# Performance work log

Measured on AMD Instinct MI355X. Metric: run time of the kernel, lower is better.

## Reference

```python
import jax, jax.numpy as jnp
import numpy as np

SR = 8                      # search_range
MO = 2 * SR + 1             # max_offset = 17
NC = MO * MO                # 289 cost-volume channels


def _l2_normalize(x, eps=1e-12):
    # torch F.normalize(p=2, dim=1): x / max(||x||_2, eps)
    n = jnp.sqrt(jnp.sum(x * x, axis=1, keepdims=True))
    return x / jnp.maximum(n, eps)


def _conv2d(x, w, b, pad, groups=1):
    out = jax.lax.conv_general_dilated(
        x, w, window_strides=(1, 1), padding=[(pad, pad), (pad, pad)],
        feature_group_count=groups,
        dimension_numbers=('NCHW', 'OIHW', 'NCHW'))
    return out + b[None, :, None, None]


def _cost_volume(x1, x2, sr, norm_both=False):
    x1 = _l2_normalize(x1)
    if norm_both:
        x2 = _l2_normalize(x2)
    bs, c, h, w = x1.shape
    padded = jnp.pad(x2, ((0, 0), (0, 0), (sr, sr), (sr, sr)))
    mo = 2 * sr + 1
    # offsets in (j outer, i inner) order, matching the original double loop
    jj, ii = jnp.meshgrid(jnp.arange(mo), jnp.arange(mo), indexing='ij')
    offs = jnp.stack([jj.reshape(-1), ii.reshape(-1)], axis=-1)  # [mo^2, 2]

    def step(carry, off):
        sl = jax.lax.dynamic_slice(padded, (0, 0, off[0], off[1]), (bs, c, h, w))
        return carry, jnp.mean(x1 * sl, axis=1)  # [bs, h, w]

    _, cv = jax.lax.scan(step, None, offs)       # [mo^2, bs, h, w]
    cv = jnp.transpose(cv, (1, 0, 2, 3))          # [bs, mo^2, h, w]
    return jax.nn.leaky_relu(cv, 0.1)


def setup_inputs() -> dict:
    key = jax.random.key(0)
    ks = jax.random.split(key, 8)
    bs, c, h, w = 4, 256, 64, 64
    scale = 0.05
    return {
        'f1': jax.random.normal(ks[0], (bs, c, h, w), jnp.float32),
        'f2': jax.random.normal(ks[1], (bs, c, h, w), jnp.float32),
        'att_w': jax.random.normal(ks[2], (NC, 1, 7, 7), jnp.float32) * scale,
        'att_b': jax.random.normal(ks[3], (NC,), jnp.float32) * scale,
        'agg1_w': jax.random.normal(ks[4], (NC // 2, NC, 3, 3), jnp.float32) * scale,
        'agg1_b': jax.random.normal(ks[5], (NC // 2,), jnp.float32) * scale,
        'agg2_w': jax.random.normal(ks[6], (49, NC // 2, 3, 3), jnp.float32) * scale,
        'agg2_b': jax.random.normal(ks[7], (49,), jnp.float32) * scale,
    }


def reference(f1, f2, att_w, att_b, agg1_w, agg1_b, agg2_w, agg2_b):
    match_vol = _cost_volume(f1, f2, SR, norm_both=False)          # [bs,289,h,w]
    att = _conv2d(match_vol, att_w, att_b, pad=3, groups=NC)       # depthwise 7x7
    att_vol = match_vol * att
    h1 = jax.nn.relu(_conv2d(att_vol, agg1_w, agg1_b, pad=1))      # Conv(289->144,3)
    out = jax.nn.relu(_conv2d(h1, agg2_w, agg2_b, pad=1))          # Conv(144->49,3)
    return out
```

## Files before the change

kernel.cpp:

```cpp
#include <hip/hip_runtime.h>
#include <hip/hip_bf16.h>

#define BS   4
#define C    256
#define HW   4096
#define NPIX 16384
#define NCH  289
#define MO   17
#define PH   80
#define PW   80
#define C1   144
#define C2   49
#define ASTR 264
#define ICP  320
#define IC3  192
#define CVP  70
#define CVC  320
#define CH64 72

typedef __bf16  bf16x8 __attribute__((ext_vector_type(8)));
typedef float   f32x4  __attribute__((ext_vector_type(4)));
typedef unsigned short us8 __attribute__((ext_vector_type(8)));

__device__ __forceinline__ void gload16(const unsigned short* g, unsigned short* l) {
    __builtin_amdgcn_global_load_lds(
        (const __attribute__((address_space(1))) unsigned int*)g,
        (__attribute__((address_space(3))) unsigned int*)l, 16, 0, 0);
}

__device__ __forceinline__ void halo_zero_dev(unsigned short* p, int H, int halo,
                                              int Cc, int blk, int t) {
    int W = H;
    int inter = H - 2 * halo;
    int total_pos = H * W - inter * inter;
    int chunks = Cc >> 3;
    size_t tot = (size_t)total_pos * chunks * BS;
    size_t idx = (size_t)blk * 256 + t;
    if (idx >= tot) return;
    int c8 = (int)(idx % chunks);
    size_t r = idx / chunks;
    int pos = (int)(r % total_pos);
    int b = (int)(r / total_pos);
    int h, w;
    int topbot = 2 * halo * W;
    if (pos < halo * W) { h = pos / W; w = pos % W; }
    else if (pos < topbot) { int q = pos - halo * W; h = H - halo + q / W; w = q % W; }
    else {
        int q = pos - topbot;
        int row = q / (2 * halo), off = q % (2 * halo);
        h = halo + row;
        w = (off < halo) ? off : (W - 2 * halo + off);
    }
    us8 z = {0, 0, 0, 0, 0, 0, 0, 0};
    *(us8*)&p[(((size_t)b * H + h) * W + w) * Cc + c8 * 8] = z;
}

__global__ void setup_kernel(unsigned short* __restrict__ x2bf, unsigned short* __restrict__ cvp,
                             unsigned short* __restrict__ avp, unsigned short* __restrict__ h1p,
                             const float* __restrict__ w1, unsigned short* __restrict__ wb1,
                             const float* __restrict__ w2, unsigned short* __restrict__ wb2,
                             const float* __restrict__ att_w, float* __restrict__ wdwp,
                             const float* __restrict__ f1, unsigned short* __restrict__ x1bf,
                             const float* __restrict__ f2) {
    __shared__ float shmem[16 * 257 + 16];
    int blk = blockIdx.x;
    int t = threadIdx.x;
    if (blk < 4030) {
        if (blk < 1152) { halo_zero_dev(x2bf, PH, 8, C, blk, t); return; }
        if (blk < 1655) { halo_zero_dev(cvp, CVP, 3, CVC, blk - 1152, t); return; }
        if (blk < 1818) { halo_zero_dev(avp, 66, 1, ICP, blk - 1655, t); return; }
        if (blk < 1916) { halo_zero_dev(h1p, 66, 1, IC3, blk - 1818, t); return; }
        if (blk < 3536) {
            int idx = (blk - 1916) * 256 + t;
            int tap = idx / (C1 * ICP);
            int r = idx - tap * (C1 * ICP);
            int oc = r / ICP;
            int ic = r - oc * ICP;
            float v = (ic < NCH) ? w1[((size_t)(oc * NCH + ic)) * 9 + tap] : 0.f;
            __hip_bfloat16 hb = __float2bfloat16(v);
            wb1[idx] = *(unsigned short*)&hb;
            return;
        }
        if (blk < 3968) {
            int idx = (blk - 3536) * 256 + t;
            int tap = idx / (64 * IC3);
            int r = idx - tap * (64 * IC3);
            int oc = r / IC3;
            int ic = r - oc * IC3;
            float v = (oc < C2 && ic < C1) ? w2[((size_t)(oc * C1 + ic)) * 9 + tap] : 0.f;
            __hip_bfloat16 hb = __float2bfloat16(v);
            wb2[idx] = *(unsigned short*)&hb;
            return;
        }
        {
            int idx = (blk - 3968) * 256 + t;
            if (idx >= 49 * CVC) return;
            int tap = idx / CVC;
            int ch = idx - tap * CVC;
            wdwp[idx] = (ch < NCH) ? att_w[ch * 49 + tap] : 0.f;
        }
        return;
    }
    if (blk < 5054) {
        float* tileT = shmem;
        float* invS = shmem + 16 * 257;
        int bb = blk - 4030;
        int pblk = bb & 255, b = bb >> 8;
        int p0 = pblk * 16;
        int tx = t & 15, ty = t >> 4;
        const float* s = f1 + (size_t)b * C * HW;
#pragma unroll
        for (int i2 = 0; i2 < 16; ++i2) {
            int c = ty + 16 * i2;
            tileT[tx * 257 + c] = s[(size_t)c * HW + p0 + tx];
        }
        __syncthreads();
        int px = t >> 4;
        int l = t & 15;
        float ssum = 0.f;
#pragma unroll
        for (int j2 = 0; j2 < 16; ++j2) {
            float v = tileT[px * 257 + l + 16 * j2];
            ssum += v * v;
        }
        ssum += __shfl_xor(ssum, 1);
        ssum += __shfl_xor(ssum, 2);
        ssum += __shfl_xor(ssum, 4);
        ssum += __shfl_xor(ssum, 8);
        if (l == 0) invS[px] = 1.0f / fmaxf(sqrtf(ssum), 1e-12f);
        __syncthreads();
#pragma unroll 4
        for (int p = 0; p < 16; ++p) {
            float v = tileT[p * 257 + t] * invS[p];
            __hip_bfloat16 hb = __float2bfloat16(v);
            x1bf[((size_t)b * HW + p0 + p) * C + t] = *(unsigned short*)&hb;
        }
        return;
    }
    {
        float* tile = shmem;
        int bb = blk - 5054;
        int pblk = bb & 127;
        int cblk = (bb >> 7) & 7;
        int b    = bb >> 10;
        int tx = t & 31, ty = t >> 5;
        int c0 = cblk * 32, p0 = pblk * 32;
        const float* s = f2 + (size_t)b * C * HW;
#pragma unroll
        for (int i = 0; i < 4; ++i) {
            int c = c0 + ty + 8 * i;
            tile[(ty + 8 * i) * 33 + tx] = s[(size_t)c * HW + p0 + tx];
        }
        __syncthreads();
#pragma unroll
        for (int i = 0; i < 4; ++i) {
            int p = p0 + ty + 8 * i;
            float v = tile[tx * 33 + ty + 8 * i];
            int c = c0 + tx;
            int h = p >> 6, w = p & 63;
            __hip_bfloat16 hb = __float2bfloat16(v);
            x2bf[(((size_t)b * PH + h + 8) * PW + (w + 8)) * C + c] = *(unsigned short*)&hb;
        }
    }
}

__global__ __launch_bounds__(512, 2)
void cv_mfma_kernel(const unsigned short* __restrict__ x1b,
                    const unsigned short* __restrict__ x2b,
                    unsigned short* __restrict__ cvp) {
    __shared__ __align__(16) unsigned short x2s[2][32 * ASTR];
    int i = blockIdx.x;
    int xcd = i & 7;
    int j = i >> 3;
    int hp = xcd * 2 + (j & 1);
    int jj = j >> 1;
    int wseg = jj & 3;
    int b = jj >> 2;
    int h0 = hp * 4;
    int w0 = wseg * 16;
    int t = threadIdx.x;
    int wave = t >> 6, lane = t & 63;
    int lrow = lane & 15, quad = lane >> 4;
    int row_w = wave >> 1, ct = wave & 1;
    int h = h0 + row_w;
    int col_l = ct * 16 + lrow;

    const unsigned short* x1p = x1b + ((size_t)b * HW + h * 64 + w0) * C;
    bf16x8 a[8];
#pragma unroll
    for (int kk = 0; kk < 8; ++kk)
        a[kk] = *(const bf16x8*)&x1p[(size_t)lrow * C + kk * 32 + quad * 8];

    const unsigned short* x2base = x2b + (size_t)b * PH * PW * C;

    {
        const unsigned short* rowp = x2base + ((size_t)h0 * PW + w0) * C;
#pragma unroll
        for (int s = 0; s < 2; ++s) {
            int v = t + s * 512;
            int col = v >> 5, ch8 = v & 31;
            *(us8*)&x2s[0][col * ASTR + ch8 * 8] = *(const us8*)&rowp[(size_t)col * C + ch8 * 8];
        }
    }
    __syncthreads();

    for (int rr = 0; rr < 20; ++rr) {
        us8 pr[2];
        bool dop = (rr + 1 < 20);
        if (dop) {
            const unsigned short* rowp = x2base + ((size_t)(h0 + rr + 1) * PW + w0) * C;
#pragma unroll
            for (int s = 0; s < 2; ++s) {
                int v = t + s * 512;
                int col = v >> 5, ch8 = v & 31;
                pr[s] = *(const us8*)&rowp[(size_t)col * C + ch8 * 8];
            }
        }

        int dj = rr - row_w;
        if ((unsigned)dj <= 16u) {
            const unsigned short* xs = x2s[rr & 1];
            f32x4 acc = {0.f, 0.f, 0.f, 0.f};
#pragma unroll
            for (int kk = 0; kk < 8; ++kk) {
                bf16x8 bb = *(const bf16x8*)&xs[col_l * ASTR + kk * 32 + quad * 8];
                acc = __builtin_amdgcn_mfma_f32_16x16x32_bf16(a[kk], bb, acc, 0, 0, 0);
            }
#pragma unroll
            for (int r = 0; r < 4; ++r) {
                int px_l = quad * 4 + r;
                int di = col_l - px_l;
                if ((unsigned)di <= 16u) {
                    float v = acc[r] * (1.0f / 256.0f);
                    v = (v > 0.f) ? v : 0.1f * v;
                    __hip_bfloat16 hb = __float2bfloat16(v);
                    cvp[(((size_t)b * CVP + h + 3) * CVP + (w0 + px_l + 3)) * CVC + dj * MO + di] =
                        *(unsigned short*)&hb;
                }
            }
        }

        if (dop) {
            unsigned short* dst = x2s[(rr + 1) & 1];
#pragma unroll
            for (int s = 0; s < 2; ++s) {
                int v = t + s * 512;
                int col = v >> 5, ch8 = v & 31;
                *(us8*)&dst[col * ASTR + ch8 * 8] = pr[s];
            }
            __syncthreads();
        }
    }
}

__global__ __launch_bounds__(256, 4)
void dw_att_tiled(const unsigned short* __restrict__ cvp,
                  const float* __restrict__ wdwp,
                  const float* __restrict__ att_b, unsigned short* __restrict__ av_pad) {
    __shared__ __align__(16) unsigned short actS[14 * 14 * 64];
    __shared__ float wdwS[49 * 64];
    int i = blockIdx.x;
    int ty = i & 7;
    int j = i >> 3;
    int cc = j % 5;
    int rest = j / 5;
    int tx = rest & 7, b = rest >> 3;
    int x0 = tx * 8, y0 = ty * 8;
    int c0 = cc * 64;
    int t = threadIdx.x;

    const unsigned short* cvb = cvp + (((size_t)b * CVP + y0) * CVP + x0) * CVC + c0;
    for (int v = t; v < 14 * 14 * 8; v += 256) {
        int rc = v >> 3, c8v = v & 7;
        int yy = rc / 14, xx = rc - yy * 14;
        *(us8*)&actS[rc * 64 + c8v * 8] =
            *(const us8*)&cvb[((size_t)yy * CVP + xx) * CVC + c8v * 8];
    }
    for (int v = t; v < 49 * 64; v += 256) {
        int tap = v >> 6, ch = v & 63;
        wdwS[v] = wdwp[tap * CVC + c0 + ch];
    }
    __syncthreads();

    int pr2 = t & 31;
    int rowg = t >> 5;
    int chl0 = 2 * pr2;
    int ch0 = c0 + chl0;
    float bv0 = (ch0 < NCH) ? att_b[ch0] : 0.f;
    float bv1 = (ch0 + 1 < NCH) ? att_b[ch0 + 1] : 0.f;
    float acc0[8], acc1[8];
#pragma unroll
    for (int px = 0; px < 8; ++px) { acc0[px] = bv0; acc1[px] = bv1; }

    for (int dy = 0; dy < 7; ++dy) {
        float w0[7], w1[7];
#pragma unroll
        for (int dx = 0; dx < 7; ++dx) {
            float2 wv = *(const float2*)&wdwS[(dy * 7 + dx) * 64 + chl0];
            w0[dx] = wv.x; w1[dx] = wv.y;
        }
        int row = rowg + dy;
        float r0[14], r1[14];
#pragma unroll
        for (int xx = 0; xx < 14; ++xx) {
            unsigned u = *(const unsigned*)&actS[(row * 14 + xx) * 64 + chl0];
            r0[xx] = __uint_as_float(u << 16);
            r1[xx] = __uint_as_float(u & 0xffff0000u);
        }
#pragma unroll
        for (int dx = 0; dx < 7; ++dx)
#pragma unroll
            for (int px = 0; px < 8; ++px) {
                acc0[px] += r0[px + dx] * w0[dx];
                acc1[px] += r1[px + dx] * w1[dx];
            }
    }

    if (ch0 < NCH) {
        bool pair = (ch0 + 1 < NCH);
#pragma unroll
        for (int px = 0; px < 8; ++px) {
            unsigned u = *(const unsigned*)&actS[((rowg + 3) * 14 + (px + 3)) * 64 + chl0];
            float c0v = __uint_as_float(u << 16);
            float c1v = __uint_as_float(u & 0xffff0000u);
            __hip_bfloat16 h0 = __float2bfloat16(c0v * acc0[px]);
            __hip_bfloat16 h1 = __float2bfloat16(c1v * acc1[px]);
            size_t o = (((size_t)b * 66 + y0 + rowg + 1) * 66 + (x0 + px + 1)) * ICP + ch0;
            if (pair) {
                unsigned ov = ((unsigned)*(unsigned short*)&h1 << 16) | (unsigned)*(unsigned short*)&h0;
                *(unsigned*)&av_pad[o] = ov;
            } else {
                av_pad[o] = *(unsigned short*)&h0;
            }
        }
    }
}

__device__ __forceinline__ const unsigned short* b1ptr(const unsigned short* wb1, int m) {
    int dy = m / 15, rm = m % 15, cc = rm / 3, dx = rm % 3;
    return wb1 + ((size_t)(dy * 3 + dx) * C1) * ICP + cc * 64;
}

__global__ __launch_bounds__(512, 2)
void agg1_mfma_kernel(const unsigned short* __restrict__ av_pad,
                      const unsigned short* __restrict__ wb1,
                      const float* __restrict__ bias,
                      unsigned short* __restrict__ h1p) {
    __shared__ __align__(16) unsigned short aS[2][72 * 64];
    __shared__ __align__(16) unsigned short bS[2][144 * 64];
    int i = blockIdx.x;
    int xcd = i & 7;
    int j = i >> 3;
    int h = xcd * 8 + (j & 7);
    int b = j >> 3;
    int t = threadIdx.x;
    int wave = t >> 6, lane = t & 63;
    int lrow = lane & 15, quad = lane >> 4;
    int og = wave & 3, mg = wave >> 2;
    int ot0 = (og == 0) ? 0 : (og * 2 + 1);
    int nt  = (og == 0) ? 3 : 2;
    int g_row = lane >> 3;
    int g_sl  = ((lane & 7) ^ g_row) << 3;

    f32x4 acc[2][3];
#pragma unroll
    for (int m = 0; m < 2; ++m)
#pragma unroll
        for (int ii = 0; ii < 3; ++ii) acc[m][ii] = (f32x4){0.f, 0.f, 0.f, 0.f};

    const unsigned short* avb = av_pad + (((size_t)b * 66 + h) * 66) * ICP;

    {
        const unsigned short* wt = b1ptr(wb1, 0);
        for (int s = wave; s < 18; s += 8)
            gload16(wt + (size_t)(s * 8 + g_row) * ICP + g_sl, &bS[0][s * 512]);
        for (int s = wave; s < 9; s += 8)
            gload16(avb + (size_t)(s * 8 + g_row) * ICP + g_sl, &aS[0][s * 512]);
    }
    __syncthreads();

    for (int k = 0; k < 45; ++k) {
        int dx = k % 3;
        if (k < 44) {
            const unsigned short* wt = b1ptr(wb1, k + 1);
            unsigned short* dst = &bS[(k + 1) & 1][0];
            for (int s = wave; s < 18; s += 8)
                gload16(wt + (size_t)(s * 8 + g_row) * ICP + g_sl, dst + s * 512);
        }
        if (dx == 0 && k < 42) {
            int p = k / 3 + 1;
            const unsigned short* ar = avb + (size_t)(p / 5) * 66 * ICP + (p % 5) * 64;
            unsigned short* dst = &aS[p & 1][0];
            for (int s = wave; s < 9; s += 8)
                gload16(ar + (size_t)(s * 8 + g_row) * ICP + g_sl, dst + s * 512);
        }
        const unsigned short* aP = aS[(k / 3) & 1];
        const unsigned short* bP = bS[k & 1];
        int swa = (lrow + dx) & 7;
        int swb = lrow & 7;
        bf16x8 afr[2][2], bfr[3][2];
#pragma unroll
        for (int c2 = 0; c2 < 2; ++c2) {
            int sl = c2 * 4 + quad;
#pragma unroll
            for (int m = 0; m < 2; ++m) {
                int P = (mg * 2 + m) * 16 + lrow + dx;
                afr[m][c2] = *(const bf16x8*)&aP[P * 64 + ((sl ^ swa) << 3)];
            }
#pragma unroll
            for (int ii = 0; ii < 3; ++ii)
                if (ii < nt) {
                    int R = (ot0 + ii) * 16 + lrow;
                    bfr[ii][c2] = *(const bf16x8*)&bP[R * 64 + ((sl ^ swb) << 3)];
                }
        }
#pragma unroll
        for (int c2 = 0; c2 < 2; ++c2)
#pragma unroll
            for (int m = 0; m < 2; ++m)
#pragma unroll
                for (int ii = 0; ii < 3; ++ii)
                    if (ii < nt)
                        acc[m][ii] = __builtin_amdgcn_mfma_f32_16x16x32_bf16(
                            afr[m][c2], bfr[ii][c2], acc[m][ii], 0, 0, 0);
        if (k < 44) __syncthreads();
    }

    size_t rowbase = ((size_t)b * 66 + h + 1) * 66;
#pragma unroll
    for (int m = 0; m < 2; ++m)
#pragma unroll
        for (int ii = 0; ii < 3; ++ii)
            if (ii < nt) {
                int oc = (ot0 + ii) * 16 + lrow;
                float bv = bias[oc];
#pragma unroll
                for (int r = 0; r < 4; ++r) {
                    int wl = (mg * 2 + m) * 16 + quad * 4 + r;
                    float val = fmaxf(acc[m][ii][r] + bv, 0.f);
                    __hip_bfloat16 hb = __float2bfloat16(val);
                    h1p[(rowbase + (wl + 1)) * IC3 + oc] = *(unsigned short*)&hb;
                }
            }
}

__device__ __forceinline__ const unsigned short* b2ptr(const unsigned short* wb2, int m) {
    int dy = m / 9, rm = m % 9, cc = rm / 3, dx = rm % 3;
    return wb2 + ((size_t)(dy * 3 + dx) * 64) * IC3 + cc * 64;
}

__global__ __launch_bounds__(256, 1)
void agg2_mfma_kernel(const unsigned short* __restrict__ h1p,
                      const unsigned short* __restrict__ wb2,
                      const float* __restrict__ bias, float* __restrict__ out) {
    __shared__ __align__(16) unsigned short aS[2][72 * 64];
    __shared__ __align__(16) unsigned short bS2[2][64 * 64];
    int i = blockIdx.x;
    int xcd = i & 7;
    int j = i >> 3;
    int h = xcd * 8 + (j & 7);
    int b = j >> 3;
    int t = threadIdx.x;
    int wave = t >> 6, lane = t & 63;
    int lrow = lane & 15, quad = lane >> 4;
    int pt = wave;
    int g_row = lane >> 3;
    int g_sl  = ((lane & 7) ^ g_row) << 3;

    f32x4 acc[4];
#pragma unroll
    for (int ot = 0; ot < 4; ++ot) acc[ot] = (f32x4){0.f, 0.f, 0.f, 0.f};

    const unsigned short* h1b = h1p + (((size_t)b * 66 + h) * 66) * IC3;

    {
        for (int s = wave; s < 8; s += 4)
            gload16(wb2 + (size_t)(s * 8 + g_row) * IC3 + g_sl, &bS2[0][s * 512]);
        for (int s = wave; s < 9; s += 4)
            gload16(h1b + (size_t)(s * 8 + g_row) * IC3 + g_sl, &aS[0][s * 512]);
    }
    __syncthreads();

    for (int k = 0; k < 27; ++k) {
        int dx = k % 3;
        if (k < 26) {
            const unsigned short* wt = b2ptr(wb2, k + 1);
            unsigned short* dst = &bS2[(k + 1) & 1][0];
            for (int s = wave; s < 8; s += 4)
                gload16(wt + (size_t)(s * 8 + g_row) * IC3 + g_sl, dst + s * 512);
        }
        if (dx == 0 && k < 24) {
            int p = k / 3 + 1;
            const unsigned short* ar = h1b + (size_t)(p / 3) * 66 * IC3 + (p % 3) * 64;
            unsigned short* dst = &aS[p & 1][0];
            for (int s = wave; s < 9; s += 4)
                gload16(ar + (size_t)(s * 8 + g_row) * IC3 + g_sl, dst + s * 512);
        }
        const unsigned short* aP = aS[(k / 3) & 1];
        const unsigned short* bP = bS2[k & 1];
        int swa = (lrow + dx) & 7;
        int swb = lrow & 7;
        bf16x8 afr[2], bfr[4][2];
#pragma unroll
        for (int c2 = 0; c2 < 2; ++c2) {
            int sl = c2 * 4 + quad;
            {
                int P = pt * 16 + lrow + dx;
                afr[c2] = *(const bf16x8*)&aP[P * 64 + ((sl ^ swa) << 3)];
            }
#pragma unroll
            for (int ot = 0; ot < 4; ++ot) {
                int R = ot * 16 + lrow;
                bfr[ot][c2] = *(const bf16x8*)&bP[R * 64 + ((sl ^ swb) << 3)];
            }
        }
#pragma unroll
        for (int c2 = 0; c2 < 2; ++c2)
#pragma unroll
            for (int ot = 0; ot < 4; ++ot)
                acc[ot] = __builtin_amdgcn_mfma_f32_16x16x32_bf16(
                    afr[c2], bfr[ot][c2], acc[ot], 0, 0, 0);
        if (k < 26) __syncthreads();
    }

#pragma unroll
    for (int ot = 0; ot < 4; ++ot) {
        int o = ot * 16 + lrow;
        if (o < C2) {
            float bv = bias[o];
#pragma unroll
            for (int r = 0; r < 4; ++r) {
                int w = pt * 16 + quad * 4 + r;
                out[((size_t)b * C2 + o) * HW + h * 64 + w] = fmaxf(acc[ot][r] + bv, 0.f);
            }
        }
    }
}

extern "C" void kernel_launch(void* const* d_in, const int* in_sizes, int n_in,
                              void* d_out, int out_size, void* d_ws, size_t ws_size,
                              hipStream_t stream) {
    const float* f1    = (const float*)d_in[0];
    const float* f2    = (const float*)d_in[1];
    const float* att_w = (const float*)d_in[2];
    const float* att_b = (const float*)d_in[3];
    const float* w1    = (const float*)d_in[4];
    const float* b1    = (const float*)d_in[5];
    const float* w2    = (const float*)d_in[6];
    const float* b2    = (const float*)d_in[7];
    float* out = (float*)d_out;

    char* wsb = (char*)d_ws;
    size_t off = 0;
    float* wdwp = (float*)(wsb + off); off += (size_t)49 * CVC * 4;
    off = (off + 15) & ~(size_t)15;
    unsigned short* x1bf = (unsigned short*)(wsb + off); off += (size_t)NPIX * C * 2;
    unsigned short* x2bf = (unsigned short*)(wsb + off); off += (size_t)BS * PH * PW * C * 2;
    unsigned short* cvp  = (unsigned short*)(wsb + off); off += (size_t)BS * CVP * CVP * CVC * 2;
    unsigned short* avp  = (unsigned short*)(wsb + off); off += (size_t)BS * 66 * 66 * ICP * 2;
    unsigned short* wb1  = (unsigned short*)(wsb + off); off += (size_t)9 * C1 * ICP * 2;
    unsigned short* h1p  = (unsigned short*)(wsb + off); off += (size_t)BS * 66 * 66 * IC3 * 2;
    unsigned short* wb2  = (unsigned short*)(wsb + off); off += (size_t)9 * 64 * IC3 * 2;
    if (ws_size < off) return;

    setup_kernel<<<9150, 256, 0, stream>>>(x2bf, cvp, avp, h1p, w1, wb1, w2, wb2,
                                           att_w, wdwp, f1, x1bf, f2);
    cv_mfma_kernel<<<256, 512, 0, stream>>>(x1bf, x2bf, cvp);
    dw_att_tiled<<<1280, 256, 0, stream>>>(cvp, wdwp, att_b, avp);
    agg1_mfma_kernel<<<256, 512, 0, stream>>>(avp, wb1, b1, h1p);
    agg2_mfma_kernel<<<256, 256, 0, stream>>>(h1p, wb2, b2, out);
}
```

Measured before the change: 191.6 us.

## Use async global-to-LDS loads with XOR swizzle in cost volume; split-K waves in agg1

The cost-volume kernel now stages x2 rows into LDS with direct global_load_lds and an XOR-swizzled layout in place of a register round-trip into a padded stride. This removes the extra VGPR staging and the separate LDS store phase, and all B fragments are loaded before the MFMA chain. The agg1 kernel switches from splitting pixels between wave groups to splitting the K dimension (channel halves) between wave groups, then reduces the partial accumulators through LDS before the epilogue. This raises the accumulator register count and adds a reduction with extra barriers, in exchange for fewer redundant B-fragment LDS reads.

```diff
diff --git a/kernel.cpp b/kernel.cpp
--- a/kernel.cpp
+++ b/kernel.cpp
@@ -11,12 +11,10 @@
 #define PW   80
 #define C1   144
 #define C2   49
-#define ASTR 264
 #define ICP  320
 #define IC3  192
 #define CVP  70
 #define CVC  320
-#define CH64 72
 
 typedef __bf16  bf16x8 __attribute__((ext_vector_type(8)));
 typedef float   f32x4  __attribute__((ext_vector_type(4)));
@@ -168,7 +166,7 @@
 void cv_mfma_kernel(const unsigned short* __restrict__ x1b,
                     const unsigned short* __restrict__ x2b,
                     unsigned short* __restrict__ cvp) {
-    __shared__ __align__(16) unsigned short x2s[2][32 * ASTR];
+    __shared__ __align__(16) unsigned short x2s[2][32 * 256];
     int i = blockIdx.x;
     int xcd = i & 7;
     int j = i >> 3;
@@ -192,40 +190,40 @@
         a[kk] = *(const bf16x8*)&x1p[(size_t)lrow * C + kk * 32 + quad * 8];
 
     const unsigned short* x2base = x2b + (size_t)b * PH * PW * C;
+    int rb = lane >> 5, sl5 = lane & 31;
 
     {
         const unsigned short* rowp = x2base + ((size_t)h0 * PW + w0) * C;
-#pragma unroll
-        for (int s = 0; s < 2; ++s) {
-            int v = t + s * 512;
-            int col = v >> 5, ch8 = v & 31;
-            *(us8*)&x2s[0][col * ASTR + ch8 * 8] = *(const us8*)&rowp[(size_t)col * C + ch8 * 8];
+        for (int s = wave; s < 16; s += 8) {
+            int r = 2 * s + rb;
+            gload16(rowp + (size_t)r * C + ((sl5 ^ (r & 7)) << 3), &x2s[0][s * 512]);
         }
     }
     __syncthreads();
 
     for (int rr = 0; rr < 20; ++rr) {
-        us8 pr[2];
         bool dop = (rr + 1 < 20);
         if (dop) {
             const unsigned short* rowp = x2base + ((size_t)(h0 + rr + 1) * PW + w0) * C;
-#pragma unroll
-            for (int s = 0; s < 2; ++s) {
-                int v = t + s * 512;
-                int col = v >> 5, ch8 = v & 31;
-                pr[s] = *(const us8*)&rowp[(size_t)col * C + ch8 * 8];
+            unsigned short* dst = &x2s[(rr + 1) & 1][0];
+            for (int s = wave; s < 16; s += 8) {
+                int r = 2 * s + rb;
+                gload16(rowp + (size_t)r * C + ((sl5 ^ (r & 7)) << 3), dst + s * 512);
             }
         }
 
         int dj = rr - row_w;
         if ((unsigned)dj <= 16u) {
             const unsigned short* xs = x2s[rr & 1];
+            bf16x8 bb[8];
+#pragma unroll
+            for (int kk = 0; kk < 8; ++kk)
+                bb[kk] = *(const bf16x8*)&xs[col_l * 256 +
+                                             (((kk * 4 + quad) ^ (col_l & 7)) << 3)];
             f32x4 acc = {0.f, 0.f, 0.f, 0.f};
 #pragma unroll
-            for (int kk = 0; kk < 8; ++kk) {
-                bf16x8 bb = *(const bf16x8*)&xs[col_l * ASTR + kk * 32 + quad * 8];
-                acc = __builtin_amdgcn_mfma_f32_16x16x32_bf16(a[kk], bb, acc, 0, 0, 0);
-            }
+            for (int kk = 0; kk < 8; ++kk)
+                acc = __builtin_amdgcn_mfma_f32_16x16x32_bf16(a[kk], bb[kk], acc, 0, 0, 0);
 #pragma unroll
             for (int r = 0; r < 4; ++r) {
                 int px_l = quad * 4 + r;
@@ -239,17 +237,7 @@
                 }
             }
         }
-
-        if (dop) {
-            unsigned short* dst = x2s[(rr + 1) & 1];
-#pragma unroll
-            for (int s = 0; s < 2; ++s) {
-                int v = t + s * 512;
-                int col = v >> 5, ch8 = v & 31;
-                *(us8*)&dst[col * ASTR + ch8 * 8] = pr[s];
-            }
-            __syncthreads();
-        }
+        if (rr < 19) __syncthreads();
     }
 }
 
@@ -356,15 +344,15 @@
     int t = threadIdx.x;
     int wave = t >> 6, lane = t & 63;
     int lrow = lane & 15, quad = lane >> 4;
-    int og = wave & 3, mg = wave >> 2;
+    int og = wave & 3, kw = wave >> 2;
     int ot0 = (og == 0) ? 0 : (og * 2 + 1);
     int nt  = (og == 0) ? 3 : 2;
     int g_row = lane >> 3;
     int g_sl  = ((lane & 7) ^ g_row) << 3;
 
-    f32x4 acc[2][3];
-#pragma unroll
-    for (int m = 0; m < 2; ++m)
+    f32x4 acc[4][3];
+#pragma unroll
+    for (int m = 0; m < 4; ++m)
 #pragma unroll
         for (int ii = 0; ii < 3; ++ii) acc[m][ii] = (f32x4){0.f, 0.f, 0.f, 0.f};
 
@@ -398,50 +386,73 @@
         const unsigned short* bP = bS[k & 1];
         int swa = (lrow + dx) & 7;
         int swb = lrow & 7;
-        bf16x8 afr[2][2], bfr[3][2];
-#pragma unroll
-        for (int c2 = 0; c2 < 2; ++c2) {
-            int sl = c2 * 4 + quad;
-#pragma unroll
-            for (int m = 0; m < 2; ++m) {
-                int P = (mg * 2 + m) * 16 + lrow + dx;
-                afr[m][c2] = *(const bf16x8*)&aP[P * 64 + ((sl ^ swa) << 3)];
-            }
+        int sl = kw * 4 + quad;
+        bf16x8 afr[4], bfr[3];
+#pragma unroll
+        for (int m = 0; m < 4; ++m) {
+            int P = m * 16 + lrow + dx;
+            afr[m] = *(const bf16x8*)&aP[P * 64 + ((sl ^ swa) << 3)];
+        }
+#pragma unroll
+        for (int ii = 0; ii < 3; ++ii)
+            if (ii < nt) {
+                int R = (ot0 + ii) * 16 + lrow;
+                bfr[ii] = *(const bf16x8*)&bP[R * 64 + ((sl ^ swb) << 3)];
+            }
+#pragma unroll
+        for (int m = 0; m < 4; ++m)
+#pragma unroll
+            for (int ii = 0; ii < 3; ++ii)
+                if (ii < nt)
+                    acc[m][ii] = __builtin_amdgcn_mfma_f32_16x16x32_bf16(
+                        afr[m], bfr[ii], acc[m][ii], 0, 0, 0);
+        if (k < 44) __syncthreads();
+    }
+
+    float4* red = (float4*)&bS[0][0];
+#pragma unroll
+    for (int p = 0; p < 4; ++p) {
+        __syncthreads();
+        if (kw == 1) {
 #pragma unroll
             for (int ii = 0; ii < 3; ++ii)
                 if (ii < nt) {
-                    int R = (ot0 + ii) * 16 + lrow;
-                    bfr[ii][c2] = *(const bf16x8*)&bP[R * 64 + ((sl ^ swb) << 3)];
+                    float4 v;
+                    v.x = acc[p][ii][0]; v.y = acc[p][ii][1];
+                    v.z = acc[p][ii][2]; v.w = acc[p][ii][3];
+                    red[(og * 3 + ii) * 64 + lane] = v;
                 }
         }
-#pragma unroll
-        for (int c2 = 0; c2 < 2; ++c2)
-#pragma unroll
-            for (int m = 0; m < 2; ++m)
-#pragma unroll
-                for (int ii = 0; ii < 3; ++ii)
-                    if (ii < nt)
-                        acc[m][ii] = __builtin_amdgcn_mfma_f32_16x16x32_bf16(
-                            afr[m][c2], bfr[ii][c2], acc[m][ii], 0, 0, 0);
-        if (k < 44) __syncthreads();
-    }
-
-    size_t rowbase = ((size_t)b * 66 + h + 1) * 66;
-#pragma unroll
-    for (int m = 0; m < 2; ++m)
-#pragma unroll
-        for (int ii = 0; ii < 3; ++ii)
-            if (ii < nt) {
-                int oc = (ot0 + ii) * 16 + lrow;
-                float bv = bias[oc];
-#pragma unroll
-                for (int r = 0; r < 4; ++r) {
-                    int wl = (mg * 2 + m) * 16 + quad * 4 + r;
-                    float val = fmaxf(acc[m][ii][r] + bv, 0.f);
-                    __hip_bfloat16 hb = __float2bfloat16(val);
-                    h1p[(rowbase + (wl + 1)) * IC3 + oc] = *(unsigned short*)&hb;
+        __syncthreads();
+        if (kw == 0) {
+#pragma unroll
+            for (int ii = 0; ii < 3; ++ii)
+                if (ii < nt) {
+                    float4 v = red[(og * 3 + ii) * 64 + lane];
+                    acc[p][ii][0] += v.x; acc[p][ii][1] += v.y;
+                    acc[p][ii][2] += v.z; acc[p][ii][3] += v.w;
                 }
-            }
+        }
+    }
+
+    if (kw == 0) {
+        size_t rowbase = ((size_t)b * 66 + h + 1) * 66;
+#pragma unroll
+        for (int m = 0; m < 4; ++m)
+#pragma unroll
+            for (int ii = 0; ii < 3; ++ii)
+                if (ii < nt) {
+                    int oc = (ot0 + ii) * 16 + lrow;
+                    float bv = bias[oc];
+#pragma unroll
+                    for (int r = 0; r < 4; ++r) {
+                        int wl = m * 16 + quad * 4 + r;
+                        float val = fmaxf(acc[m][ii][r] + bv, 0.f);
+                        __hip_bfloat16 hb = __float2bfloat16(val);
+                        h1p[(rowbase + (wl + 1)) * IC3 + oc] = *(unsigned short*)&hb;
+                    }
+                }
+    }
 }
 
 __device__ __forceinline__ const unsigned short* b2ptr(const unsigned short* wb2, int m) {
```

Result: no change. 192.2 us (+0.3%).
